# Optimization experiments

Measured on AMD Instinct MI355X. Metric: run time of the kernel, lower is better.

Reference implementation:

```python
import jax, jax.numpy as jnp
import numpy as np

WS = 7          # window size
SHIFT = WS // 2 # shift for odd blocks
NH = 8          # num heads
EPS = 1e-5


def _rel_pos_index(ws):
    coords = np.stack(np.meshgrid(np.arange(ws), np.arange(ws), indexing='ij'))  # (2, ws, ws)
    cf = coords.reshape(2, -1)                                  # (2, N)
    rc = (cf[:, :, None] - cf[:, None, :]).transpose(1, 2, 0)   # (N, N, 2)
    rc[..., 0] += ws - 1
    rc[..., 1] += ws - 1
    rc[..., 0] *= 2 * ws - 1
    return rc.sum(-1)  # (N, N) int


def _attn_mask(Hp, Wp, ws, shift):
    # (nW, N, N) additive mask with 0 / -100, as in the torch code
    img = np.zeros((Hp, Wp), dtype=np.float32)
    cnt = 0
    slices = (slice(0, -ws), slice(-ws, -shift), slice(-shift, None))
    for h in slices:
        for w in slices:
            img[h, w] = cnt
            cnt += 1
    mw = img.reshape(Hp // ws, ws, Wp // ws, ws).transpose(0, 2, 1, 3).reshape(-1, ws * ws)
    am = mw[:, None, :] - mw[:, :, None]
    return np.where(am != 0, -100.0, 0.0).astype(np.float32)


def _layernorm(x, w, b):
    m = x.mean(-1, keepdims=True)
    v = ((x - m) ** 2).mean(-1, keepdims=True)
    return (x - m) * jax.lax.rsqrt(v + EPS) * w + b


def _window_partition(x, ws):
    B, H, W, C = x.shape
    x = x.reshape(B, H // ws, ws, W // ws, ws, C).transpose(0, 1, 3, 2, 4, 5)
    return x.reshape(-1, ws * ws, C)


def _window_reverse(w, ws, H, W):
    B = w.shape[0] // (H // ws * W // ws)
    x = w.reshape(B, H // ws, W // ws, ws, ws, -1).transpose(0, 1, 3, 2, 4, 5)
    return x.reshape(B, H, W, -1)


def _window_msa(xw, qkv_w, qkv_b, proj_w, proj_b, rpb, rel_idx, mask):
    Bw, N, C = xw.shape
    hd = C // NH
    qkv = (xw @ qkv_w.T + qkv_b).reshape(Bw, N, 3, NH, hd).transpose(2, 0, 3, 1, 4)
    q, k, v = qkv[0] * (hd ** -0.5), qkv[1], qkv[2]
    attn = jnp.einsum('bhnd,bhmd->bhnm', q, k)                      # (Bw, NH, N, N)
    bias = rpb[rel_idx.reshape(-1)].reshape(N, N, NH).transpose(2, 0, 1)
    attn = attn + bias[None]
    if mask is not None:
        nW = mask.shape[0]
        attn = attn.reshape(Bw // nW, nW, NH, N, N) + mask[None, :, None]
        attn = attn.reshape(Bw, NH, N, N)
    attn = jax.nn.softmax(attn, axis=-1)
    out = jnp.einsum('bhnm,bhmd->bhnd', attn, v).transpose(0, 2, 1, 3).reshape(Bw, N, C)
    return out @ proj_w.T + proj_b


def _forward(x, ln1_w, ln1_b, qkv_w, qkv_b, proj_w, proj_b, rpb,
             ln2_w, ln2_b, mlp_w1, mlp_b1, mlp_w2, mlp_b2, H, W):
    B, L, C = x.shape
    rel_idx = _rel_pos_index(WS)
    pad_r = (WS - W % WS) % WS
    pad_b = (WS - H % WS) % WS
    Hp, Wp = H + pad_b, W + pad_r
    depth = ln1_w.shape[0]
    for i in range(depth):
        shift = 0 if i % 2 == 0 else SHIFT
        shortcut = x
        h = _layernorm(x, ln1_w[i], ln1_b[i]).reshape(B, H, W, C)
        if pad_r > 0 or pad_b > 0:
            h = jnp.pad(h, ((0, 0), (0, pad_b), (0, pad_r), (0, 0)))
        if shift > 0:
            h = jnp.roll(h, (-shift, -shift), axis=(1, 2))
            mask = jnp.asarray(_attn_mask(Hp, Wp, WS, shift))
        else:
            mask = None
        hw = _window_partition(h, WS)
        hw = _window_msa(hw, qkv_w[i], qkv_b[i], proj_w[i], proj_b[i], rpb[i], rel_idx, mask)
        h = _window_reverse(hw.reshape(-1, WS, WS, C), WS, Hp, Wp)
        if shift > 0:
            h = jnp.roll(h, (shift, shift), axis=(1, 2))
        if pad_r > 0 or pad_b > 0:
            h = h[:, :H, :W, :]
        x = shortcut + h.reshape(B, H * W, C)
        m = _layernorm(x, ln2_w[i], ln2_b[i])
        m = jax.nn.gelu(m @ mlp_w1[i].T + mlp_b1[i], approximate=False)
        x = x + (m @ mlp_w2[i].T + mlp_b2[i])
    return x


def setup_inputs() -> dict:
    key = jax.random.key(0)
    ks = jax.random.split(key, 8)
    B, H, W, C, D = 8, 112, 112, 256, 2
    hid = 4 * C
    return {
        'x': jax.random.normal(ks[0], (B, H * W, C), jnp.float32),
        'ln1_w': jnp.ones((D, C), jnp.float32),
        'ln1_b': jnp.zeros((D, C), jnp.float32),
        'qkv_w': jax.random.normal(ks[1], (D, 3 * C, C), jnp.float32) * 0.02,
        'qkv_b': jnp.zeros((D, 3 * C), jnp.float32),
        'proj_w': jax.random.normal(ks[2], (D, C, C), jnp.float32) * 0.02,
        'proj_b': jnp.zeros((D, C), jnp.float32),
        'rpb': jax.random.normal(ks[3], (D, (2 * WS - 1) ** 2, NH), jnp.float32) * 0.02,
        'ln2_w': jnp.ones((D, C), jnp.float32),
        'ln2_b': jnp.zeros((D, C), jnp.float32),
        'mlp_w1': jax.random.normal(ks[4], (D, hid, C), jnp.float32) * 0.02,
        'mlp_b1': jnp.zeros((D, hid), jnp.float32),
        'mlp_w2': jax.random.normal(ks[5], (D, C, hid), jnp.float32) * 0.02,
        'mlp_b2': jnp.zeros((D, C), jnp.float32),
        'H': H,
        'W': W,
    }


def reference(x, ln1_w, ln1_b, qkv_w, qkv_b, proj_w, proj_b, rpb,
              ln2_w, ln2_b, mlp_w1, mlp_b1, mlp_w2, mlp_b2, H, W):
    return _forward(x, ln1_w, ln1_b, qkv_w, qkv_b, proj_w, proj_b, rpb,
                    ln2_w, ln2_b, mlp_w1, mlp_b1, mlp_w2, mlp_b2, H, W)
```

## Files before the change

kernel.cpp:

```cpp
#include <hip/hip_runtime.h>

typedef unsigned short u16;
typedef unsigned int u32;
typedef __attribute__((ext_vector_type(8))) short bf16x8;
typedef __attribute__((ext_vector_type(4))) float f32x4;
typedef __attribute__((ext_vector_type(16))) float f32x16;
typedef __attribute__((ext_vector_type(8))) unsigned short u16x8;
typedef const __attribute__((address_space(1))) void gvoid;
typedef __attribute__((address_space(3))) void svoid;

#define T_TOK 100352
#define CDIM 256
#define ATTN_SCALE 0.17677669529663687f

__device__ __forceinline__ u16 f2bf(float f) {
    u32 u = __float_as_uint(f);
    u32 r = (u + 0x7fffu + ((u >> 16) & 1u)) >> 16;
    return (u16)r;
}
__device__ __forceinline__ float bf2f(u16 h) {
    return __uint_as_float(((u32)h) << 16);
}
__device__ __forceinline__ float gelu_f(float x) {
    float z = 0.7978845608028654f * (x + 0.044715f * x * x * x);
    float e = __expf(2.0f * z);
    float th = 1.0f - 2.0f * __builtin_amdgcn_rcpf(e + 1.0f);
    return 0.5f * x * (1.0f + th);
}
__device__ __forceinline__ int div7(int q) { return (q * 37) >> 8; }
__device__ __forceinline__ int reg3(int r) { return r < 105 ? 0 : (r < 109 ? 1 : 2); }

__global__ void cvt_kernel(const float* __restrict__ in, u16* __restrict__ out, int n) {
    int i = blockIdx.x * 256 + threadIdx.x;
    if (i < n) out[i] = f2bf(in[i]);
}

__global__ __launch_bounds__(256) void ln_kernel(
    const float* __restrict__ X, const float* __restrict__ w,
    const float* __restrict__ b, u16* __restrict__ Y)
{
    int wid = threadIdx.x >> 6, l = threadIdx.x & 63;
    int t = blockIdx.x * 4 + wid;
    const float4 x4 = ((const float4*)(X + (size_t)t * CDIM))[l];
    float s  = x4.x + x4.y + x4.z + x4.w;
    float s2 = x4.x*x4.x + x4.y*x4.y + x4.z*x4.z + x4.w*x4.w;
    #pragma unroll
    for (int o = 32; o; o >>= 1) { s += __shfl_xor(s, o); s2 += __shfl_xor(s2, o); }
    float mean = s * (1.0f/256.0f);
    float var  = s2 * (1.0f/256.0f) - mean*mean;
    float rstd = rsqrtf(var + 1e-5f);
    float4 w4 = ((const float4*)w)[l];
    float4 b4 = ((const float4*)b)[l];
    ushort4 o4;
    o4.x = f2bf((x4.x - mean)*rstd*w4.x + b4.x);
    o4.y = f2bf((x4.y - mean)*rstd*w4.y + b4.y);
    o4.z = f2bf((x4.z - mean)*rstd*w4.z + b4.z);
    o4.w = f2bf((x4.w - mean)*rstd*w4.w + b4.w);
    ((ushort4*)(Y + (size_t)t * CDIM))[l] = o4;
}

template<int EPI>
__global__ __launch_bounds__(256) void gemm_kernel(
    const u16* __restrict__ A, const u16* __restrict__ Bw,
    const float* __restrict__ bias, void* __restrict__ outp,
    const float* __restrict__ res, int N, int K, int nTn)
{
    __shared__ __align__(16) char lds_raw[69632];
    u16 (*lds)[2][128 * 64] = (u16(*)[2][128 * 64])lds_raw;
    const int tid = threadIdx.x;
    const int l = tid & 63;
    const int w = tid >> 6;
    const int wr = w >> 1, wc = w & 1;

    const int nBlocks = gridDim.x;
    const int cpx = nBlocks >> 3;
    const int lin = (blockIdx.x & 7) * cpx + (blockIdx.x >> 3);
    const int nT = lin % nTn;
    const int mT = lin / nTn;

    f32x4 acc[4][4];
    #pragma unroll
    for (int m = 0; m < 4; ++m)
        #pragma unroll
        for (int n = 0; n < 4; ++n) acc[m][n] = (f32x4){0.f,0.f,0.f,0.f};

    const int sr = tid >> 3;
    const int sg = tid & 7;

    #define STAGE(buf, kt)                                                              \
        {                                                                               \
            _Pragma("unroll")                                                           \
            for (int c = 0; c < 4; ++c) {                                               \
                int r = c*32 + sr;                                                      \
                int gsrc = sg ^ (r & 7);                                                \
                const u16* ga = A  + (size_t)(mT*128 + r) * K + (kt) + gsrc*8;          \
                const u16* gb = Bw + (size_t)(nT*128 + r) * K + (kt) + gsrc*8;          \
                u16* la = &lds[buf][0][(c*256 + w*64) * 8];                              \
                u16* lb = &lds[buf][1][(c*256 + w*64) * 8];                              \
                __builtin_amdgcn_global_load_lds((gvoid*)ga, (svoid*)la, 16, 0, 0);     \
                __builtin_amdgcn_global_load_lds((gvoid*)gb, (svoid*)lb, 16, 0, 0);     \
            }                                                                           \
        }

    const int nSteps = K >> 6;
    int cur = 0;

    STAGE(0, 0);
    asm volatile("s_waitcnt vmcnt(0)" ::: "memory");
    __builtin_amdgcn_s_barrier();
    asm volatile("" ::: "memory");

    const int lr = l & 15, gq = l >> 4;
    for (int t = 0; t < nSteps; ++t) {
        bf16x8 a[2][4], b[2][4];
        #pragma unroll
        for (int kk = 0; kk < 2; ++kk) {
            #pragma unroll
            for (int m = 0; m < 4; ++m) {
                int r = wr*64 + m*16 + lr;
                int g = kk*4 + gq;
                a[kk][m] = *(const bf16x8*)&lds[cur][0][r*64 + (g ^ (r & 7))*8];
            }
            #pragma unroll
            for (int n = 0; n < 4; ++n) {
                int r = wc*64 + n*16 + lr;
                int g = kk*4 + gq;
                b[kk][n] = *(const bf16x8*)&lds[cur][1][r*64 + (g ^ (r & 7))*8];
            }
        }
        if (t + 1 < nSteps) STAGE(cur ^ 1, (t + 1) * 64);

        __builtin_amdgcn_s_setprio(1);
        #pragma unroll
        for (int kk = 0; kk < 2; ++kk)
            #pragma unroll
            for (int m = 0; m < 4; ++m)
                #pragma unroll
                for (int n = 0; n < 4; ++n)
                    acc[m][n] = __builtin_amdgcn_mfma_f32_16x16x32_bf16(a[kk][m], b[kk][n], acc[m][n], 0, 0, 0);
        __builtin_amdgcn_s_setprio(0);

        asm volatile("s_waitcnt vmcnt(0)" ::: "memory");
        __builtin_amdgcn_s_barrier();
        asm volatile("" ::: "memory");
        cur ^= 1;
    }
    #undef STAGE

    if (EPI == 2) {
        float* epf = (float*)lds_raw + w * (64 * 68);
        #pragma unroll
        for (int m = 0; m < 4; ++m)
            #pragma unroll
            for (int n = 0; n < 4; ++n) {
                float bb = bias[nT*128 + wc*64 + n*16 + lr];
                #pragma unroll
                for (int j = 0; j < 4; ++j)
                    epf[(m*16 + gq*4 + j)*68 + n*16 + lr] = acc[m][n][j] + bb;
            }
        const int rr4 = l >> 4, cc4 = (l & 15) * 4;
        float* outf = (float*)outp;
        #pragma unroll
        for (int p = 0; p < 16; ++p) {
            float4 vv = *(const float4*)&epf[(p*4 + rr4)*68 + cc4];
            size_t grow = (size_t)(mT*128 + wr*64 + p*4 + rr4);
            size_t gcol = (size_t)(nT*128 + wc*64 + cc4);
            float4 rv = *(const float4*)(res + grow*N + gcol);
            float4 ov; ov.x = vv.x + rv.x; ov.y = vv.y + rv.y;
            ov.z = vv.z + rv.z; ov.w = vv.w + rv.w;
            *(float4*)(outf + grow*N + gcol) = ov;
        }
    } else {
        u16* ep = (u16*)lds_raw + w * (64 * 72);
        #pragma unroll
        for (int m = 0; m < 4; ++m)
            #pragma unroll
            for (int n = 0; n < 4; ++n) {
                float bb = bias[nT*128 + wc*64 + n*16 + lr];
                #pragma unroll
                for (int j = 0; j < 4; ++j) {
                    float v = acc[m][n][j] + bb;
                    if (EPI == 1) v = gelu_f(v);
                    ep[(m*16 + gq*4 + j)*72 + n*16 + lr] = f2bf(v);
                }
            }
        const int rr8 = l >> 3, cc8 = (l & 7) * 8;
        u16* outw = (u16*)outp;
        #pragma unroll
        for (int p = 0; p < 8; ++p) {
            u16x8 vv = *(const u16x8*)&ep[(p*8 + rr8)*72 + cc8];
            size_t grow = (size_t)(mT*128 + wr*64 + p*8 + rr8);
            size_t gcol = (size_t)(nT*128 + wc*64 + cc8);
            *(u16x8*)(outw + grow*N + gcol) = vv;
        }
    }
}

__global__ __launch_bounds__(256) void attn_kernel(
    const u16* __restrict__ qkv, const float* __restrict__ rpb,
    u16* __restrict__ outb, int shift)
{
    __shared__ u16 Vt[8][2048];
    __shared__ float biasl[8 * 176];
    __shared__ int tok[64];

    const int t = threadIdx.x;
    const int w = t >> 6;
    const int l = t & 63;
    const int lo = l & 31;
    const int hi = l >> 5;
    const int win = blockIdx.x;
    const int wj = win & 15, wi = (win >> 4) & 15, bb = win >> 8;

    if (t < 64) {
        int qq = t > 48 ? 48 : t;
        int i = div7(qq), j = qq - i*7;
        int rr = wi*7 + i + shift; if (rr >= 112) rr -= 112;
        int cc = wj*7 + j + shift; if (cc >= 112) cc -= 112;
        tok[t] = bb*12544 + rr*112 + cc;
    }
    for (int i2 = t; i2 < 1352; i2 += 256)
        biasl[(i2 & 7)*176 + (i2 >> 3)] = rpb[i2];
    __syncthreads();

    int iqv[2], jqv[2], regq[2];
    #pragma unroll
    for (int nt = 0; nt < 2; ++nt) {
        int q = nt*32 + lo; int qb = q > 48 ? 48 : q;
        int iq = div7(qb), jq = qb - iq*7;
        iqv[nt] = iq; jqv[nt] = jq;
        regq[nt] = 0;
        if (shift > 0) regq[nt] = reg3(wi*7 + iq)*3 + reg3(wj*7 + jq);
    }

    #pragma unroll 1
    for (int hh = 0; hh < 2; ++hh) {
        const int h = 2*w + hh;

        {
            u16x8 vreg[4];
            if (l < 49) {
                const u16x8* vs = (const u16x8*)(qkv + (size_t)tok[l]*768 + 512 + h*32);
                #pragma unroll
                for (int c4 = 0; c4 < 4; ++c4) vreg[c4] = vs[c4];
            } else {
                #pragma unroll
                for (int c4 = 0; c4 < 4; ++c4) vreg[c4] = (u16x8){0,0,0,0,0,0,0,0};
            }
            u16* vt = &Vt[h][0];
            #pragma unroll
            for (int c4 = 0; c4 < 4; ++c4)
                #pragma unroll
                for (int e = 0; e < 8; ++e)
                    vt[(c4*8 + e)*64 + (l ^ (e << 3))] = vreg[c4][e];
        }

        bf16x8 kf[2][2], qf[2][2];
        #pragma unroll
        for (int mt = 0; mt < 2; ++mt)
            #pragma unroll
            for (int td = 0; td < 2; ++td)
                kf[mt][td] = *(const bf16x8*)(qkv + (size_t)tok[mt*32 + lo]*768 + 256 + h*32 + td*16 + hi*8);
        #pragma unroll
        for (int nt = 0; nt < 2; ++nt)
            #pragma unroll
            for (int td = 0; td < 2; ++td)
                qf[nt][td] = *(const bf16x8*)(qkv + (size_t)tok[nt*32 + lo]*768 + h*32 + td*16 + hi*8);

        f32x16 s[2][2];
        #pragma unroll
        for (int mt = 0; mt < 2; ++mt)
            #pragma unroll
            for (int nt = 0; nt < 2; ++nt) {
                f32x16 z;
                #pragma unroll
                for (int i = 0; i < 16; ++i) z[i] = 0.f;
                s[mt][nt] = z;
            }
        #pragma unroll
        for (int td = 0; td < 2; ++td)
            #pragma unroll
            for (int mt = 0; mt < 2; ++mt)
                #pragma unroll
                for (int nt = 0; nt < 2; ++nt)
                    s[mt][nt] = __builtin_amdgcn_mfma_f32_32x32x16_bf16(kf[mt][td], qf[nt][td], s[mt][nt], 0, 0, 0);

        asm volatile("s_waitcnt lgkmcnt(0)" ::: "memory");
        __builtin_amdgcn_sched_barrier(0);

        const float* bh = biasl + h*176;
        #pragma unroll
        for (int mt = 0; mt < 2; ++mt) {
            #pragma unroll
            for (int i = 0; i < 16; ++i) {
                int r = (i & 3) + 8*(i >> 2) + 4*hi;
                int k = mt*32 + r;
                bool valid = k < 49;
                int kb = valid ? k : 48;
                int ik = div7(kb), jk = kb - ik*7;
                int regk = 0;
                if (shift > 0) regk = reg3(wi*7 + ik)*3 + reg3(wj*7 + jk);
                #pragma unroll
                for (int nt = 0; nt < 2; ++nt) {
                    float v = s[mt][nt][i] * ATTN_SCALE
                            + bh[(iqv[nt] - ik + 6)*13 + (jqv[nt] - jk + 6)];
                    if (shift > 0 && regq[nt] != regk) v -= 100.0f;
                    if (!valid) v = -1e30f;
                    s[mt][nt][i] = v;
                }
            }
        }

        #pragma unroll
        for (int nt = 0; nt < 2; ++nt) {
            float mx = -1e30f;
            #pragma unroll
            for (int i = 0; i < 16; ++i) mx = fmaxf(mx, fmaxf(s[0][nt][i], s[1][nt][i]));
            mx = fmaxf(mx, __shfl_xor(mx, 32));
            float sum = 0.f;
            #pragma unroll
            for (int mt = 0; mt < 2; ++mt)
                #pragma unroll
                for (int i = 0; i < 16; ++i) {
                    float e = __expf(s[mt][nt][i] - mx);
                    s[mt][nt][i] = e;
                    sum += e;
                }
            sum += __shfl_xor(sum, 32);
            float inv = __builtin_amdgcn_rcpf(sum);

            u32 pk[2][8];
            #pragma unroll
            for (int mt = 0; mt < 2; ++mt)
                #pragma unroll
                for (int j = 0; j < 8; ++j)
                    pk[mt][j] = (u32)f2bf(s[mt][nt][2*j] * inv)
                              | ((u32)f2bf(s[mt][nt][2*j + 1] * inv) << 16);

            f32x16 o;
            #pragma unroll
            for (int i = 0; i < 16; ++i) o[i] = 0.f;
            #pragma unroll
            for (int kt = 0; kt < 4; ++kt) {
                const int mt = kt >> 1;
                const int base = (kt & 1) * 4;
                u32 a0 = pk[mt][base + 0], a1 = pk[mt][base + 1];
                u32 a2 = pk[mt][base + 2], a3 = pk[mt][base + 3];
                asm volatile("v_permlane32_swap_b32 %0, %1" : "+v"(a0), "+v"(a2));
                asm volatile("v_permlane32_swap_b32 %0, %1" : "+v"(a1), "+v"(a3));
                union { u32 u[4]; bf16x8 v; } pf;
                pf.u[0] = a0; pf.u[1] = a1; pf.u[2] = a2; pf.u[3] = a3;
                bf16x8 vb = *(const bf16x8*)(&Vt[h][lo*64 + ((kt*16 + hi*8) ^ ((lo & 7) << 3))]);
                o = __builtin_amdgcn_mfma_f32_32x32x16_bf16(pf.v, vb, o, 0, 0, 0);
            }

            #pragma unroll
            for (int i = 0; i < 16; ++i) {
                int q = nt*32 + (i & 3) + 8*(i >> 2) + 4*hi;
                if (q < 49)
                    outb[(size_t)tok[q]*256 + h*32 + lo] = f2bf(o[i]);
            }
        }
    }
}

extern "C" void kernel_launch(void* const* d_in, const int* in_sizes, int n_in,
                              void* d_out, int out_size, void* d_ws, size_t ws_size,
                              hipStream_t stream) {
    const float* x_in   = (const float*)d_in[0];
    const float* ln1_w  = (const float*)d_in[1];
    const float* ln1_b  = (const float*)d_in[2];
    const float* qkv_w  = (const float*)d_in[3];
    const float* qkv_b  = (const float*)d_in[4];
    const float* proj_w = (const float*)d_in[5];
    const float* proj_b = (const float*)d_in[6];
    const float* rpb    = (const float*)d_in[7];
    const float* ln2_w  = (const float*)d_in[8];
    const float* ln2_b  = (const float*)d_in[9];
    const float* mlp_w1 = (const float*)d_in[10];
    const float* mlp_b1 = (const float*)d_in[11];
    const float* mlp_w2 = (const float*)d_in[12];
    const float* mlp_b2 = (const float*)d_in[13];
    float* xout = (float*)d_out;

    char* p = (char*)d_ws;
    u16* wq = (u16*)p;  p += (size_t)2*768*256*2;
    u16* wp = (u16*)p;  p += (size_t)2*256*256*2;
    u16* w1 = (u16*)p;  p += (size_t)2*1024*256*2;
    u16* w2 = (u16*)p;  p += (size_t)2*256*1024*2;
    u16* buf_y   = (u16*)p; p += (size_t)T_TOK*256*2;
    u16* buf_big = (u16*)p;

    {
        int n;
        n = 2*768*256;  cvt_kernel<<<(n+255)/256, 256, 0, stream>>>(qkv_w,  wq, n);
        n = 2*256*256;  cvt_kernel<<<(n+255)/256, 256, 0, stream>>>(proj_w, wp, n);
        n = 2*1024*256; cvt_kernel<<<(n+255)/256, 256, 0, stream>>>(mlp_w1, w1, n);
        n = 2*256*1024; cvt_kernel<<<(n+255)/256, 256, 0, stream>>>(mlp_w2, w2, n);
    }

    for (int i = 0; i < 2; ++i) {
        const int shift = (i == 0) ? 0 : 3;
        const float* xcur = (i == 0) ? x_in : xout;

        ln_kernel<<<T_TOK/4, 256, 0, stream>>>(xcur, ln1_w + i*256, ln1_b + i*256, buf_y);
        gemm_kernel<0><<<784*6, 256, 0, stream>>>(
            buf_y, wq + (size_t)i*768*256, qkv_b + i*768, buf_big, nullptr, 768, 256, 6);
        attn_kernel<<<2048, 256, 0, stream>>>(buf_big, rpb + i*169*8, buf_y, shift);
        gemm_kernel<2><<<784*2, 256, 0, stream>>>(
            buf_y, wp + (size_t)i*256*256, proj_b + i*256, xout, xcur, 256, 256, 2);
        ln_kernel<<<T_TOK/4, 256, 0, stream>>>(xout, ln2_w + i*256, ln2_b + i*256, buf_y);
        gemm_kernel<1><<<784*8, 256, 0, stream>>>(
            buf_y, w1 + (size_t)i*1024*256, mlp_b1 + i*1024, buf_big, nullptr, 1024, 256, 8);
        gemm_kernel<2><<<784*2, 256, 0, stream>>>(
            buf_big, w2 + (size_t)i*256*1024, mlp_b2 + i*256, xout, xout, 256, 1024, 2);
    }
}
```

Baseline: 1.001 ms.

## Fuse LayerNorm into residual GEMM epilogues with full-row tiles

Adds a GEMM kernel whose block covers all 256 output columns for 128 rows. That lets it add the residual, compute per-row LayerNorm statistics through shuffles and shared memory, and write the normalized bf16 activations for the next stage. This removes three of the four standalone LayerNorm launches and their extra fp32 reads of the residual stream. The bf16 epilogue in the existing GEMM now stages fp32 in LDS and packs with a hardware bf16 convert instruction. The fused kernel uses fewer, larger blocks with more accumulators per thread, which may reduce occupancy and parallelism. It also reads back the output it just wrote to global memory.

```diff
diff --git a/kernel.cpp b/kernel.cpp
--- a/kernel.cpp
+++ b/kernel.cpp
@@ -6,6 +6,7 @@
 typedef __attribute__((ext_vector_type(4))) float f32x4;
 typedef __attribute__((ext_vector_type(16))) float f32x16;
 typedef __attribute__((ext_vector_type(8))) unsigned short u16x8;
+typedef __attribute__((ext_vector_type(2))) unsigned int u32x2;
 typedef const __attribute__((address_space(1))) void gvoid;
 typedef __attribute__((address_space(3))) void svoid;
 
@@ -20,6 +21,11 @@
 }
 __device__ __forceinline__ float bf2f(u16 h) {
     return __uint_as_float(((u32)h) << 16);
+}
+__device__ __forceinline__ u32 cvtpk(float lo, float hi) {
+    u32 r;
+    asm("v_cvt_pk_bf16_f32 %0, %1, %2" : "=v"(r) : "v"(lo), "v"(hi));
+    return r;
 }
 __device__ __forceinline__ float gelu_f(float x) {
     float z = 0.7978845608028654f * (x + 0.044715f * x * x * x);
@@ -171,7 +177,7 @@
             *(float4*)(outf + grow*N + gcol) = ov;
         }
     } else {
-        u16* ep = (u16*)lds_raw + w * (64 * 72);
+        float* epf = (float*)lds_raw + w * (64 * 68);
         #pragma unroll
         for (int m = 0; m < 4; ++m)
             #pragma unroll
@@ -181,18 +187,177 @@
                 for (int j = 0; j < 4; ++j) {
                     float v = acc[m][n][j] + bb;
                     if (EPI == 1) v = gelu_f(v);
-                    ep[(m*16 + gq*4 + j)*72 + n*16 + lr] = f2bf(v);
+                    epf[(m*16 + gq*4 + j)*68 + n*16 + lr] = v;
                 }
             }
         const int rr8 = l >> 3, cc8 = (l & 7) * 8;
         u16* outw = (u16*)outp;
         #pragma unroll
         for (int p = 0; p < 8; ++p) {
-            u16x8 vv = *(const u16x8*)&ep[(p*8 + rr8)*72 + cc8];
+            float4 v0 = *(const float4*)&epf[(p*8 + rr8)*68 + cc8];
+            float4 v1 = *(const float4*)&epf[(p*8 + rr8)*68 + cc8 + 4];
+            union { u32 u[4]; u16x8 v; } pk;
+            pk.u[0] = cvtpk(v0.x, v0.y); pk.u[1] = cvtpk(v0.z, v0.w);
+            pk.u[2] = cvtpk(v1.x, v1.y); pk.u[3] = cvtpk(v1.z, v1.w);
             size_t grow = (size_t)(mT*128 + wr*64 + p*8 + rr8);
             size_t gcol = (size_t)(nT*128 + wc*64 + cc8);
-            *(u16x8*)(outw + grow*N + gcol) = vv;
-        }
+            *(u16x8*)(outw + grow*N + gcol) = pk.v;
+        }
+    }
+}
+
+__global__ __launch_bounds__(256, 2) void gemm_ln_kernel(
+    const u16* __restrict__ A, const u16* __restrict__ Bw,
+    const float* __restrict__ bias, float* __restrict__ xoutp,
+    const float* __restrict__ res, const float* __restrict__ lnw,
+    const float* __restrict__ lnb, u16* __restrict__ yout, int K)
+{
+    __shared__ __align__(16) char lds_raw[74752];
+    float (*stats)[4][2] = (float(*)[4][2])(lds_raw + 69632);
+    float2* ln_ms = (float2*)(lds_raw + 73728);
+
+    const int tid = threadIdx.x;
+    const int l = tid & 63;
+    const int w = tid >> 6;
+    const int wr = w >> 1, wc = w & 1;
+    const int lr = l & 15, gq = l >> 4;
+
+    const int mT = (blockIdx.x & 7) * 98 + (blockIdx.x >> 3);
+
+    f32x4 acc[2][4][4];
+    #pragma unroll
+    for (int nh = 0; nh < 2; ++nh)
+        #pragma unroll
+        for (int m = 0; m < 4; ++m)
+            #pragma unroll
+            for (int n = 0; n < 4; ++n) acc[nh][m][n] = (f32x4){0.f,0.f,0.f,0.f};
+
+    #define STG(buf, kt)                                                                 \
+        {                                                                                \
+            _Pragma("unroll")                                                            \
+            for (int c = 0; c < 6; ++c) {                                                \
+                int idx = c*256 + tid;                                                   \
+                int li  = (c < 2) ? idx : idx - 512;                                     \
+                int rp = li >> 3, uu = li & 7;                                           \
+                int v2 = uu ^ (rp & 7);                                                  \
+                int r  = rp*2 + (v2 >> 2);                                               \
+                int g  = v2 & 3;                                                         \
+                const u16* gs = (c < 2) ? (A + (size_t)(mT*128 + r)*K + (kt) + g*8)      \
+                                        : (Bw + (size_t)r*K + (kt) + g*8);               \
+                u16* ld = (u16*)(lds_raw + (buf)*24576 +                                 \
+                    ((c < 2) ? (c*256 + w*64)*16 : 8192 + ((c-2)*256 + w*64)*16));       \
+                __builtin_amdgcn_global_load_lds((gvoid*)gs, (svoid*)ld, 16, 0, 0);      \
+            }                                                                            \
+        }
+
+    const int nSteps = K >> 5;
+    int cur = 0;
+
+    STG(0, 0);
+    asm volatile("s_waitcnt vmcnt(0)" ::: "memory");
+    __builtin_amdgcn_s_barrier();
+    asm volatile("" ::: "memory");
+
+    for (int t = 0; t < nSteps; ++t) {
+        const char* bA = lds_raw + cur*24576;
+        const char* bB = bA + 8192;
+        bf16x8 a[4], b[2][4];
+        #pragma unroll
+        for (int m = 0; m < 4; ++m) {
+            int r = wr*64 + m*16 + lr;
+            int rp = r >> 1, s = (((r & 1) << 2) | gq) ^ (rp & 7);
+            a[m] = *(const bf16x8*)(bA + rp*128 + s*16);
+        }
+        #pragma unroll
+        for (int nh = 0; nh < 2; ++nh)
+            #pragma unroll
+            for (int n = 0; n < 4; ++n) {
+                int r = nh*128 + wc*64 + n*16 + lr;
+                int rp = r >> 1, s = (((r & 1) << 2) | gq) ^ (rp & 7);
+                b[nh][n] = *(const bf16x8*)(bB + rp*128 + s*16);
+            }
+        if (t + 1 < nSteps) STG(cur ^ 1, (t + 1) * 32);
+
+        __builtin_amdgcn_s_setprio(1);
+        #pragma unroll
+        for (int nh = 0; nh < 2; ++nh)
+            #pragma unroll
+            for (int m = 0; m < 4; ++m)
+                #pragma unroll
+                for (int n = 0; n < 4; ++n)
+                    acc[nh][m][n] = __builtin_amdgcn_mfma_f32_16x16x32_bf16(a[m], b[nh][n], acc[nh][m][n], 0, 0, 0);
+        __builtin_amdgcn_s_setprio(0);
+
+        asm volatile("s_waitcnt vmcnt(0)" ::: "memory");
+        __builtin_amdgcn_s_barrier();
+        asm volatile("" ::: "memory");
+        cur ^= 1;
+    }
+    #undef STG
+
+    float* scr = (float*)(lds_raw + w * 17408);
+    const int rr4 = l >> 4, cc4 = (l & 15) * 4;
+    #pragma unroll
+    for (int nh = 0; nh < 2; ++nh) {
+        #pragma unroll
+        for (int m = 0; m < 4; ++m)
+            #pragma unroll
+            for (int n = 0; n < 4; ++n) {
+                float bb = bias[nh*128 + wc*64 + n*16 + lr];
+                #pragma unroll
+                for (int j = 0; j < 4; ++j)
+                    scr[(m*16 + gq*4 + j)*68 + n*16 + lr] = acc[nh][m][n][j] + bb;
+            }
+        #pragma unroll
+        for (int p = 0; p < 16; ++p) {
+            int lrow = wr*64 + p*4 + rr4;
+            float4 vv = *(const float4*)&scr[(p*4 + rr4)*68 + cc4];
+            size_t off = (size_t)(mT*128 + lrow) * 256 + nh*128 + wc*64 + cc4;
+            float4 rv = *(const float4*)(res + off);
+            float4 ov; ov.x = vv.x + rv.x; ov.y = vv.y + rv.y;
+            ov.z = vv.z + rv.z; ov.w = vv.w + rv.w;
+            *(float4*)(xoutp + off) = ov;
+            float s  = (ov.x + ov.y) + (ov.z + ov.w);
+            float s2 = (ov.x*ov.x + ov.y*ov.y) + (ov.z*ov.z + ov.w*ov.w);
+            s  += __shfl_xor(s, 1);  s  += __shfl_xor(s, 2);
+            s  += __shfl_xor(s, 4);  s  += __shfl_xor(s, 8);
+            s2 += __shfl_xor(s2, 1); s2 += __shfl_xor(s2, 2);
+            s2 += __shfl_xor(s2, 4); s2 += __shfl_xor(s2, 8);
+            if ((l & 15) == 0) {
+                stats[lrow][nh*2 + wc][0] = s;
+                stats[lrow][nh*2 + wc][1] = s2;
+            }
+        }
+    }
+    __syncthreads();
+
+    if (tid < 128) {
+        float s = 0.f, s2 = 0.f;
+        #pragma unroll
+        for (int q = 0; q < 4; ++q) { s += stats[tid][q][0]; s2 += stats[tid][q][1]; }
+        float mean = s * (1.0f/256.0f);
+        float var  = s2 * (1.0f/256.0f) - mean*mean;
+        float2 ms; ms.x = mean; ms.y = rsqrtf(var + 1e-5f);
+        ln_ms[tid] = ms;
+    }
+    __syncthreads();
+
+    const int col = (tid & 63) * 4;
+    const float4 w4 = *(const float4*)(lnw + col);
+    const float4 b4 = *(const float4*)(lnb + col);
+    #pragma unroll
+    for (int p = 0; p < 32; ++p) {
+        int lrow = p*4 + w;
+        float2 ms = ln_ms[lrow];
+        size_t off = (size_t)(mT*128 + lrow) * 256 + col;
+        float4 xv = *(const float4*)(xoutp + off);
+        float r0 = (xv.x - ms.x)*ms.y*w4.x + b4.x;
+        float r1 = (xv.y - ms.x)*ms.y*w4.y + b4.y;
+        float r2 = (xv.z - ms.x)*ms.y*w4.z + b4.z;
+        float r3 = (xv.w - ms.x)*ms.y*w4.w + b4.w;
+        union { u32 u[2]; u32x2 v; } pk;
+        pk.u[0] = cvtpk(r0, r1); pk.u[1] = cvtpk(r2, r3);
+        *(u32x2*)(yout + off) = pk.v;
     }
 }
 
@@ -399,20 +564,24 @@
         n = 2*256*1024; cvt_kernel<<<(n+255)/256, 256, 0, stream>>>(mlp_w2, w2, n);
     }
 
-    for (int i = 0; i < 2; ++i) {
-        const int shift = (i == 0) ? 0 : 3;
-        const float* xcur = (i == 0) ? x_in : xout;
-
-        ln_kernel<<<T_TOK/4, 256, 0, stream>>>(xcur, ln1_w + i*256, ln1_b + i*256, buf_y);
-        gemm_kernel<0><<<784*6, 256, 0, stream>>>(
-            buf_y, wq + (size_t)i*768*256, qkv_b + i*768, buf_big, nullptr, 768, 256, 6);
-        attn_kernel<<<2048, 256, 0, stream>>>(buf_big, rpb + i*169*8, buf_y, shift);
-        gemm_kernel<2><<<784*2, 256, 0, stream>>>(
-            buf_y, wp + (size_t)i*256*256, proj_b + i*256, xout, xcur, 256, 256, 2);
-        ln_kernel<<<T_TOK/4, 256, 0, stream>>>(xout, ln2_w + i*256, ln2_b + i*256, buf_y);
-        gemm_kernel<1><<<784*8, 256, 0, stream>>>(
-            buf_y, w1 + (size_t)i*1024*256, mlp_b1 + i*1024, buf_big, nullptr, 1024, 256, 8);
-        gemm_kernel<2><<<784*2, 256, 0, stream>>>(
-            buf_big, w2 + (size_t)i*256*1024, mlp_b2 + i*256, xout, xout, 256, 1024, 2);
-    }
-}
+    ln_kernel<<<T_TOK/4, 256, 0, stream>>>(x_in, ln1_w, ln1_b, buf_y);
+    gemm_kernel<0><<<784*6, 256, 0, stream>>>(
+        buf_y, wq, qkv_b, buf_big, nullptr, 768, 256, 6);
+    attn_kernel<<<2048, 256, 0, stream>>>(buf_big, rpb, buf_y, 0);
+    gemm_ln_kernel<<<784, 256, 0, stream>>>(
+        buf_y, wp, proj_b, xout, x_in, ln2_w, ln2_b, buf_y, 256);
+    gemm_kernel<1><<<784*8, 256, 0, stream>>>(
+        buf_y, w1, mlp_b1, buf_big, nullptr, 1024, 256, 8);
+    gemm_ln_kernel<<<784, 256, 0, stream>>>(
+        buf_big, w2, mlp_b2, xout, xout, ln1_w + 256, ln1_b + 256, buf_y, 1024);
+
+    gemm_kernel<0><<<784*6, 256, 0, stream>>>(
+        buf_y, wq + (size_t)768*256, qkv_b + 768, buf_big, nullptr, 768, 256, 6);
+    attn_kernel<<<2048, 256, 0, stream>>>(buf_big, rpb + 169*8, buf_y, 3);
+    gemm_ln_kernel<<<784, 256, 0, stream>>>(
+        buf_y, wp + (size_t)256*256, proj_b + 256, xout, xout, ln2_w + 256, ln2_b + 256, buf_y, 256);
+    gemm_kernel<1><<<784*8, 256, 0, stream>>>(
+        buf_y, w1 + (size_t)1024*256, mlp_b1 + 1024, buf_big, nullptr, 1024, 256, 8);
+    gemm_kernel<2><<<784*2, 256, 0, stream>>>(
+        buf_big, w2 + (size_t)256*1024, mlp_b2 + 256, xout, xout, 256, 1024, 2);
+}
```

Result: slower. 1.057 ms (+5.6%).

## Fuse MLP fc1+GELU+fc2 into one kernel keeping hidden activations on-chip

Applied to the files above, without the earlier changes.

Adds an mlp_kernel where each block computes 128 rows of fc1 in 32-wide hidden chunks, applies bias and GELU in registers, repacks the result into MFMA operand layout with permlane32 swaps, and accumulates fc2 directly. Weight chunks are double-buffered in LDS via global_load_lds. This removes the write and re-read of the 100k x 1024 bf16 hidden tensor and one kernel launch per block. The generic GEMM epilogue also switches to packed hardware bf16 conversion. In exchange, the fused kernel holds large register accumulators and the Y fragments, which limits occupancy, and it has only 784 blocks.

```diff
diff --git a/kernel.cpp b/kernel.cpp
--- a/kernel.cpp
+++ b/kernel.cpp
@@ -20,6 +20,11 @@
 }
 __device__ __forceinline__ float bf2f(u16 h) {
     return __uint_as_float(((u32)h) << 16);
+}
+__device__ __forceinline__ u32 cvtpk(float lo, float hi) {
+    u32 r;
+    asm("v_cvt_pk_bf16_f32 %0, %1, %2" : "=v"(r) : "v"(lo), "v"(hi));
+    return r;
 }
 __device__ __forceinline__ float gelu_f(float x) {
     float z = 0.7978845608028654f * (x + 0.044715f * x * x * x);
@@ -171,7 +176,7 @@
             *(float4*)(outf + grow*N + gcol) = ov;
         }
     } else {
-        u16* ep = (u16*)lds_raw + w * (64 * 72);
+        float* epf = (float*)lds_raw + w * (64 * 68);
         #pragma unroll
         for (int m = 0; m < 4; ++m)
             #pragma unroll
@@ -181,18 +186,167 @@
                 for (int j = 0; j < 4; ++j) {
                     float v = acc[m][n][j] + bb;
                     if (EPI == 1) v = gelu_f(v);
-                    ep[(m*16 + gq*4 + j)*72 + n*16 + lr] = f2bf(v);
+                    epf[(m*16 + gq*4 + j)*68 + n*16 + lr] = v;
                 }
             }
         const int rr8 = l >> 3, cc8 = (l & 7) * 8;
         u16* outw = (u16*)outp;
         #pragma unroll
         for (int p = 0; p < 8; ++p) {
-            u16x8 vv = *(const u16x8*)&ep[(p*8 + rr8)*72 + cc8];
+            float4 v0 = *(const float4*)&epf[(p*8 + rr8)*68 + cc8];
+            float4 v1 = *(const float4*)&epf[(p*8 + rr8)*68 + cc8 + 4];
+            union { u32 u[4]; u16x8 v; } pk;
+            pk.u[0] = cvtpk(v0.x, v0.y); pk.u[1] = cvtpk(v0.z, v0.w);
+            pk.u[2] = cvtpk(v1.x, v1.y); pk.u[3] = cvtpk(v1.z, v1.w);
             size_t grow = (size_t)(mT*128 + wr*64 + p*8 + rr8);
             size_t gcol = (size_t)(nT*128 + wc*64 + cc8);
-            *(u16x8*)(outw + grow*N + gcol) = vv;
-        }
+            *(u16x8*)(outw + grow*N + gcol) = pk.v;
+        }
+    }
+}
+
+__global__ __launch_bounds__(256, 2) void mlp_kernel(
+    const u16* __restrict__ Y, const u16* __restrict__ W1,
+    const float* __restrict__ B1, const u16* __restrict__ W2,
+    const float* __restrict__ B2, const float* __restrict__ res,
+    float* __restrict__ xout)
+{
+    __shared__ __align__(16) char lds_raw[69632];
+
+    const int tid = threadIdx.x;
+    const int l = tid & 63;
+    const int w = tid >> 6;
+    const int lo = l & 31;
+    const int hi = l >> 5;
+    const int row0 = blockIdx.x * 128 + w * 32;
+
+    bf16x8 yf[16];
+    #pragma unroll
+    for (int kt = 0; kt < 16; ++kt)
+        yf[kt] = *(const bf16x8*)(Y + (size_t)(row0 + lo) * 256 + kt*16 + hi*8);
+
+    float b2v[8];
+    #pragma unroll
+    for (int ot = 0; ot < 8; ++ot) b2v[ot] = B2[ot*32 + lo];
+
+    ((float4*)(lds_raw + 65536))[tid] = ((const float4*)B1)[tid];
+
+    f32x16 acc[8];
+    #pragma unroll
+    for (int ot = 0; ot < 8; ++ot) {
+        f32x16 z;
+        #pragma unroll
+        for (int i = 0; i < 16; ++i) z[i] = 0.f;
+        acc[ot] = z;
+    }
+
+    const int w1r = tid >> 5;
+    const int w1s = tid & 31;
+    const int w2r = tid >> 2;
+    const int w2g = (tid & 3) ^ ((tid >> 2) & 3);
+
+    #define MSTG(buf, ch)                                                                  \
+        {                                                                                  \
+            _Pragma("unroll")                                                              \
+            for (int c = 0; c < 4; ++c) {                                                  \
+                int r1 = c*8 + w1r;                                                        \
+                const u16* g1 = W1 + (size_t)((ch)*32 + r1)*256 + (w1s ^ r1)*8;            \
+                u16* d1 = (u16*)(lds_raw + (buf)*32768 + (c*256 + w*64)*16);               \
+                __builtin_amdgcn_global_load_lds((gvoid*)g1, (svoid*)d1, 16, 0, 0);        \
+                const u16* g2 = W2 + (size_t)(c*64 + w2r)*1024 + (ch)*32 + w2g*8;          \
+                u16* d2 = (u16*)(lds_raw + (buf)*32768 + 16384 + (c*256 + w*64)*16);       \
+                __builtin_amdgcn_global_load_lds((gvoid*)g2, (svoid*)d2, 16, 0, 0);        \
+            }                                                                              \
+        }
+
+    MSTG(0, 0);
+    __syncthreads();
+
+    #pragma unroll 1
+    for (int ch = 0; ch < 32; ++ch) {
+        const int cur = ch & 1;
+        const char* w1b = lds_raw + cur*32768;
+        const char* w2b = w1b + 16384;
+
+        f32x16 ht;
+        #pragma unroll
+        for (int i = 0; i < 16; ++i) ht[i] = 0.f;
+        #pragma unroll
+        for (int kt = 0; kt < 16; ++kt) {
+            int slot = (2*kt + hi) ^ lo;
+            bf16x8 w1f = *(const bf16x8*)(w1b + lo*512 + slot*16);
+            ht = __builtin_amdgcn_mfma_f32_32x32x16_bf16(w1f, yf[kt], ht, 0, 0, 0);
+        }
+
+        if (ch + 1 < 32) MSTG(cur ^ 1, ch + 1);
+
+        const float* b1l = (const float*)(lds_raw + 65536) + ch*32;
+        #pragma unroll
+        for (int i = 0; i < 16; ++i) {
+            int r = (i & 3) + 8*(i >> 2) + 4*hi;
+            ht[i] = gelu_f(ht[i] + b1l[r]);
+        }
+
+        u32 pk[8];
+        #pragma unroll
+        for (int j = 0; j < 8; ++j) pk[j] = cvtpk(ht[2*j], ht[2*j+1]);
+        bf16x8 pa[2];
+        #pragma unroll
+        for (int s2 = 0; s2 < 2; ++s2) {
+            u32 a0 = pk[s2*4 + 0], a1 = pk[s2*4 + 1];
+            u32 a2 = pk[s2*4 + 2], a3 = pk[s2*4 + 3];
+            asm volatile("v_permlane32_swap_b32 %0, %1" : "+v"(a0), "+v"(a2));
+            asm volatile("v_permlane32_swap_b32 %0, %1" : "+v"(a1), "+v"(a3));
+            union { u32 u[4]; bf16x8 v; } pf;
+            pf.u[0] = a0; pf.u[1] = a1; pf.u[2] = a2; pf.u[3] = a3;
+            pa[s2] = pf.v;
+        }
+
+        __builtin_amdgcn_s_setprio(1);
+        #pragma unroll
+        for (int ot = 0; ot < 8; ++ot) {
+            #pragma unroll
+            for (int ks = 0; ks < 2; ++ks) {
+                int r = ot*32 + lo;
+                int slot = (2*ks + hi) ^ (r & 3);
+                bf16x8 w2f = *(const bf16x8*)(w2b + r*64 + slot*16);
+                acc[ot] = __builtin_amdgcn_mfma_f32_32x32x16_bf16(pa[ks], w2f, acc[ot], 0, 0, 0);
+            }
+        }
+        __builtin_amdgcn_s_setprio(0);
+
+        asm volatile("s_waitcnt vmcnt(0)" ::: "memory");
+        __builtin_amdgcn_s_barrier();
+        asm volatile("" ::: "memory");
+    }
+    #undef MSTG
+
+    float* scr = (float*)(lds_raw + w * 16640);
+    #pragma unroll 1
+    for (int half = 0; half < 2; ++half) {
+        #pragma unroll
+        for (int ot4 = 0; ot4 < 4; ++ot4) {
+            int ot = half*4 + ot4;
+            #pragma unroll
+            for (int i = 0; i < 16; ++i) {
+                int r = (i & 3) + 8*(i >> 2) + 4*hi;
+                scr[r*130 + ot4*32 + lo] = acc[ot][i] + b2v[ot];
+            }
+        }
+        asm volatile("s_waitcnt lgkmcnt(0)" ::: "memory");
+        __builtin_amdgcn_sched_barrier(0);
+        const int rr = l >> 5, cc = (l & 31) * 4;
+        #pragma unroll
+        for (int p = 0; p < 16; ++p) {
+            float4 vv = *(const float4*)&scr[(p*2 + rr)*130 + cc];
+            size_t off = (size_t)(row0 + p*2 + rr) * 256 + half*128 + cc;
+            float4 rv = *(const float4*)(res + off);
+            float4 ov; ov.x = vv.x + rv.x; ov.y = vv.y + rv.y;
+            ov.z = vv.z + rv.z; ov.w = vv.w + rv.w;
+            *(float4*)(xout + off) = ov;
+        }
+        asm volatile("s_waitcnt lgkmcnt(0)" ::: "memory");
+        __builtin_amdgcn_sched_barrier(0);
     }
 }
 
@@ -410,9 +564,8 @@
         gemm_kernel<2><<<784*2, 256, 0, stream>>>(
             buf_y, wp + (size_t)i*256*256, proj_b + i*256, xout, xcur, 256, 256, 2);
         ln_kernel<<<T_TOK/4, 256, 0, stream>>>(xout, ln2_w + i*256, ln2_b + i*256, buf_y);
-        gemm_kernel<1><<<784*8, 256, 0, stream>>>(
-            buf_y, w1 + (size_t)i*1024*256, mlp_b1 + i*1024, buf_big, nullptr, 1024, 256, 8);
-        gemm_kernel<2><<<784*2, 256, 0, stream>>>(
-            buf_big, w2 + (size_t)i*256*1024, mlp_b2 + i*256, xout, xout, 256, 1024, 2);
-    }
-}
+        mlp_kernel<<<784, 256, 0, stream>>>(
+            buf_y, w1 + (size_t)i*1024*256, mlp_b1 + i*1024,
+            w2 + (size_t)i*256*1024, mlp_b2 + i*256, xout, xout);
+    }
+}
```

New measurement: 959.9 us. 4.1% less time.
